# Kernel tuning notes

Measured on AMD Instinct MI355X. Metric: run time of the kernel, lower is better.

Reference implementation:

```python
import jax, jax.numpy as jnp
import numpy as np

B, D, K = 32, 20000, 16
HH, EH, L, DH = 128, 256, 32, 128


def setup_inputs() -> dict:
    key = jax.random.key(0)
    ks = jax.random.split(key, 16)
    g = lambda k, shape, fan_in: jax.random.normal(k, shape, jnp.float32) / np.sqrt(fan_in)
    return {
        "x": jax.random.normal(ks[0], (B, D), jnp.float32),
        "mask": jax.random.randint(ks[1], (B, D), 0, 2, jnp.int32),
        # encoder feature embedding/bias (shared with decoder)
        "F_embed": jax.random.normal(ks[2], (D, K), jnp.float32),
        "f_bias": jnp.zeros((D, 1), jnp.float32),
        # h_layer: Linear(1+K+1 -> HH), Linear(HH -> K)
        "W1": g(ks[3], (2 + K, HH), 2 + K), "b1": jnp.zeros((HH,), jnp.float32),
        "W2": g(ks[4], (HH, K), HH), "b2": jnp.zeros((K,), jnp.float32),
        # encoder_mlp: Linear(K -> EH), Linear(EH -> 2L)
        "We1": g(ks[5], (K, EH), K), "be1": jnp.zeros((EH,), jnp.float32),
        "We2": g(ks[6], (EH, 2 * L), EH), "be2": jnp.zeros((2 * L,), jnp.float32),
        # z_processor: Linear(L -> DH)
        "Wz": g(ks[7], (L, DH), L), "bz": jnp.zeros((DH,), jnp.float32),
        # j_layer: Linear(DH+K+1 -> DH), Linear(DH -> 1)
        "Wj1": g(ks[8], (DH + K + 1, DH), DH + K + 1), "bj1": jnp.zeros((DH,), jnp.float32),
        "Wj2": g(ks[9], (DH, 1), DH), "bj2": jnp.zeros((1,), jnp.float32),
    }


def reference(x, mask, F_embed, f_bias, W1, b1, W2, b2, We1, be1, We2, be2,
              Wz, bz, Wj1, bj1, Wj2, bj2):
    relu = jax.nn.relu
    bsz = x.shape[0]
    # ---- encoder: per-feature shared h_layer ----
    # h_input = [x_j, F_j, b_j] : (B, D, 2+K)
    h_in = jnp.concatenate([
        x[:, :, None],
        jnp.broadcast_to(F_embed[None], (bsz, D, K)),
        jnp.broadcast_to(f_bias[None], (bsz, D, 1)),
    ], axis=-1)
    h = relu(h_in @ W1 + b1)          # (B, D, HH)
    h = relu(h @ W2 + b2)             # (B, D, K)
    c = jnp.sum(h * mask.astype(jnp.float32)[:, :, None], axis=1)  # (B, K)
    enc = relu(c @ We1 + be1) @ We2 + be2                          # (B, 2L)
    mu, logvar = enc[:, :L], enc[:, L:]
    # eval mode: z = mu
    z = mu
    # ---- decoder: broadcast-concat shared j_layer ----
    pz = relu(z @ Wz + bz)            # (B, DH)
    j_in = jnp.concatenate([
        jnp.broadcast_to(pz[:, None, :], (bsz, D, DH)),
        jnp.broadcast_to(F_embed[None], (bsz, D, K)),
        jnp.broadcast_to(f_bias[None], (bsz, D, 1)),
    ], axis=-1)                       # (B, D, DH+K+1)
    rec = (relu(j_in @ Wj1 + bj1) @ Wj2 + bj2)[..., 0]  # (B, D)
    return rec, mu, logvar
```

## Files before the change

kernel.cpp:

```cpp
#include <hip/hip_runtime.h>

#define Dn 20000
#define Bn 32


__global__ __launch_bounds__(256) void kA1(const float* __restrict__ F_embed,
                                           const float* __restrict__ f_bias,
                                           const float* __restrict__ W1,
                                           const float* __restrict__ b1,
                                           float* __restrict__ F1)
{
    const int t  = threadIdx.x;
    const int k  = t & 127;
    const int dl = t >> 7;
    const int d0 = blockIdx.x * 8;
    float w[17];
#pragma unroll
    for (int i = 0; i < 16; ++i) w[i] = W1[(1 + i) * 128 + k];
    w[16] = W1[17 * 128 + k];
    const float bb = b1[k];
#pragma unroll
    for (int r = 0; r < 4; ++r) {
        const int d = d0 + r * 2 + dl;
        float acc = fmaf(f_bias[d], w[16], bb);
#pragma unroll
        for (int i = 0; i < 16; ++i) acc = fmaf(F_embed[d * 16 + i], w[i], acc);
        F1[d * 128 + k] = acc;
    }
}

__global__ __launch_bounds__(256) void kA2(const float* __restrict__ F_embed,
                                           const float* __restrict__ f_bias,
                                           const float* __restrict__ Wj1,
                                           float* __restrict__ FjT)
{
    const int d  = blockIdx.x * 256 + threadIdx.x;
    const int kg = blockIdx.y * 8;
    if (d >= Dn) return;
    const float4* fe4 = (const float4*)(F_embed + d * 16);
    float fe[16];
    {
        float4 a = fe4[0], b = fe4[1], c = fe4[2], e = fe4[3];
        fe[0]=a.x; fe[1]=a.y; fe[2]=a.z; fe[3]=a.w;
        fe[4]=b.x; fe[5]=b.y; fe[6]=b.z; fe[7]=b.w;
        fe[8]=c.x; fe[9]=c.y; fe[10]=c.z; fe[11]=c.w;
        fe[12]=e.x; fe[13]=e.y; fe[14]=e.z; fe[15]=e.w;
    }
    const float fb = f_bias[d];
#pragma unroll
    for (int j = 0; j < 8; ++j) {
        const int k = kg + j;
        float acc = fb * Wj1[144 * 128 + k];
#pragma unroll
        for (int i = 0; i < 16; ++i) acc = fmaf(fe[i], Wj1[(128 + i) * 128 + k], acc);
        FjT[k * Dn + d] = acc;
    }
}

__global__ __launch_bounds__(256) void kB(const float* __restrict__ x,
                                          const int* __restrict__ mask,
                                          const float* __restrict__ F1,
                                          const float* __restrict__ W1,
                                          const float* __restrict__ W2,
                                          const float* __restrict__ b2,
                                          float* __restrict__ partial)
{
    const int t   = threadIdx.x;
    const int b   = t & 31;
    const int dsl = t >> 5;
    const int d   = blockIdx.x * 8 + dsl;

    const float xv = x[b * Dn + d];
    const float m  = (float)mask[b * Dn + d];

    float acc[16];
#pragma unroll
    for (int j = 0; j < 16; ++j) acc[j] = 0.f;

    const float4* f14 = (const float4*)(F1 + d * 128);
#pragma unroll 8
    for (int k4 = 0; k4 < 32; ++k4) {
        const float4 f = f14[k4];
        const float h0 = fmaxf(fmaf(xv, W1[k4 * 4 + 0], f.x), 0.f);
        const float h1 = fmaxf(fmaf(xv, W1[k4 * 4 + 1], f.y), 0.f);
        const float h2 = fmaxf(fmaf(xv, W1[k4 * 4 + 2], f.z), 0.f);
        const float h3 = fmaxf(fmaf(xv, W1[k4 * 4 + 3], f.w), 0.f);
#pragma unroll
        for (int j = 0; j < 16; ++j) {
            float a = acc[j];
            a = fmaf(h0, W2[(k4 * 4 + 0) * 16 + j], a);
            a = fmaf(h1, W2[(k4 * 4 + 1) * 16 + j], a);
            a = fmaf(h2, W2[(k4 * 4 + 2) * 16 + j], a);
            a = fmaf(h3, W2[(k4 * 4 + 3) * 16 + j], a);
            acc[j] = a;
        }
    }
#pragma unroll
    for (int j = 0; j < 16; ++j) acc[j] = m * fmaxf(acc[j] + b2[j], 0.f);

#pragma unroll
    for (int j = 0; j < 16; ++j) acc[j] += __shfl_xor(acc[j], 32);
    __shared__ float red[4][544];
    const int wv   = t >> 6;
    const int lane = t & 63;
    if (lane < 32) {
#pragma unroll
        for (int j = 0; j < 16; ++j) red[wv][b * 17 + j] = acc[j];
    }
    __syncthreads();
    float* __restrict__ po = partial + blockIdx.x * 512;
    for (int o = t; o < 512; o += 256) {
        const int ob = o >> 4, oj = o & 15;
        const int idx = ob * 17 + oj;
        po[o] = red[0][idx] + red[1][idx] + red[2][idx] + red[3][idx];
    }
}

__global__ __launch_bounds__(256) void kR(const float* __restrict__ partial,
                                          float* __restrict__ cws)
{
    const int o  = blockIdx.x * 256 + threadIdx.x;
    const int r0 = blockIdx.y * 250;
    float s = 0.f;
#pragma unroll 5
    for (int r = 0; r < 250; ++r) s += partial[(r0 + r) * 512 + o];
    atomicAdd(cws + o, s);
}

__global__ __launch_bounds__(256) void kC(const float* __restrict__ cws,
                                          const float* __restrict__ We1,
                                          const float* __restrict__ be1,
                                          const float* __restrict__ We2,
                                          const float* __restrict__ be2,
                                          const float* __restrict__ Wz,
                                          const float* __restrict__ bz,
                                          const float* __restrict__ Wj1,
                                          const float* __restrict__ bj1,
                                          float* __restrict__ out,
                                          float* __restrict__ basews)
{
    const int b = blockIdx.x;
    const int t = threadIdx.x;
    __shared__ float cb[16];
    __shared__ float henc[256];
    __shared__ float ep[4][64];
    __shared__ float zl[32];
    __shared__ float pzl[128];
    __shared__ float jp[2][128];

    if (t < 16) cb[t] = cws[b * 16 + t];
    __syncthreads();

    {
        float a = be1[t];
#pragma unroll
        for (int i = 0; i < 16; ++i) a = fmaf(cb[i], We1[i * 256 + t], a);
        henc[t] = fmaxf(a, 0.f);
    }
    __syncthreads();

    {
        const int o = t & 63, s = t >> 6;
        float a = 0.f;
#pragma unroll 8
        for (int i = 0; i < 64; ++i) a = fmaf(henc[s * 64 + i], We2[(s * 64 + i) * 64 + o], a);
        ep[s][o] = a;
    }
    __syncthreads();
    if (t < 64) {
        const float e = be2[t] + ep[0][t] + ep[1][t] + ep[2][t] + ep[3][t];
        if (t < 32) { out[640000 + b * 32 + t] = e; zl[t] = e; }
        else        { out[641024 + b * 32 + (t - 32)] = e; }
    }
    __syncthreads();

    if (t < 128) {
        float a = bz[t];
#pragma unroll 8
        for (int i = 0; i < 32; ++i) a = fmaf(zl[i], Wz[i * 128 + t], a);
        pzl[t] = fmaxf(a, 0.f);
    }
    __syncthreads();

    {
        const int k = t & 127, s = t >> 7;
        float a = 0.f;
#pragma unroll 8
        for (int i = 0; i < 64; ++i) a = fmaf(pzl[s * 64 + i], Wj1[(s * 64 + i) * 128 + k], a);
        jp[s][k] = a;
    }
    __syncthreads();
    if (t < 128) basews[b * 128 + t] = bj1[t] + jp[0][t] + jp[1][t];
}

__global__ __launch_bounds__(256) void kD(const float* __restrict__ FjT,
                                          const float* __restrict__ basews,
                                          const float* __restrict__ Wj2,
                                          const float* __restrict__ bj2,
                                          float* __restrict__ rec)
{
    const int d  = blockIdx.x * 256 + threadIdx.x;
    const int bq = blockIdx.y * 4;
    if (d >= Dn) return;
    const float* __restrict__ bA = basews + (bq + 0) * 128;
    const float* __restrict__ bB = basews + (bq + 1) * 128;
    const float* __restrict__ bC = basews + (bq + 2) * 128;
    const float* __restrict__ bD = basews + (bq + 3) * 128;
    float a0 = 0.f, a1 = 0.f, a2 = 0.f, a3 = 0.f;
#pragma unroll 8
    for (int k = 0; k < 128; ++k) {
        const float fj = FjT[k * Dn + d];
        const float w  = Wj2[k];
        a0 = fmaf(fmaxf(fj + bA[k], 0.f), w, a0);
        a1 = fmaf(fmaxf(fj + bB[k], 0.f), w, a1);
        a2 = fmaf(fmaxf(fj + bC[k], 0.f), w, a2);
        a3 = fmaf(fmaxf(fj + bD[k], 0.f), w, a3);
    }
    const float bj = bj2[0];
    rec[(bq + 0) * Dn + d] = a0 + bj;
    rec[(bq + 1) * Dn + d] = a1 + bj;
    rec[(bq + 2) * Dn + d] = a2 + bj;
    rec[(bq + 3) * Dn + d] = a3 + bj;
}

extern "C" void kernel_launch(void* const* d_in, const int* in_sizes, int n_in,
                              void* d_out, int out_size, void* d_ws, size_t ws_size,
                              hipStream_t stream)
{
    const float* x       = (const float*)d_in[0];
    const int*   mask    = (const int*)d_in[1];
    const float* F_embed = (const float*)d_in[2];
    const float* f_bias  = (const float*)d_in[3];
    const float* W1      = (const float*)d_in[4];
    const float* b1      = (const float*)d_in[5];
    const float* W2      = (const float*)d_in[6];
    const float* b2      = (const float*)d_in[7];
    const float* We1     = (const float*)d_in[8];
    const float* be1     = (const float*)d_in[9];
    const float* We2     = (const float*)d_in[10];
    const float* be2     = (const float*)d_in[11];
    const float* Wz      = (const float*)d_in[12];
    const float* bz      = (const float*)d_in[13];
    const float* Wj1     = (const float*)d_in[14];
    const float* bj1     = (const float*)d_in[15];
    const float* Wj2     = (const float*)d_in[16];
    const float* bj2     = (const float*)d_in[17];
    float* out = (float*)d_out;
    float* ws  = (float*)d_ws;

    float* F1      = ws;
    float* FjT     = ws + 2560000;
    float* partial = ws + 2560000;
    float* cws     = ws + 5120000;
    float* basews  = ws + 5120512;

    hipMemsetAsync(cws, 0, 512 * sizeof(float), stream);
    kA1<<<2500, 256, 0, stream>>>(F_embed, f_bias, W1, b1, F1);
    kB<<<2500, 256, 0, stream>>>(x, mask, F1, W1, W2, b2, partial);
    kR<<<dim3(2, 10), 256, 0, stream>>>(partial, cws);
    kC<<<32, 256, 0, stream>>>(cws, We1, be1, We2, be2, Wz, bz, Wj1, bj1, out, basews);
    kA2<<<dim3(79, 16), 256, 0, stream>>>(F_embed, f_bias, Wj1, FjT);
    kD<<<dim3(79, 8), 256, 0, stream>>>(FjT, basews, Wj2, bj2, out);
}
```

Baseline: 189.9 us.

## Use bf16 MFMA for encoder h-layer second matmul in kB

Rewrites the encoder kernel kB so the HH->K second layer runs on bf16 16x16x32 MFMA instructions instead of scalar FP32 FMAs. Each block now covers 16 features with x and mask staged in shared memory, so the grid and the kR reduction extents are halved. This removes most of the scalar FMA work in the largest compute stage, at the cost of bf16 rounding of the hidden activations and W2.

```diff
diff --git a/kernel.cpp b/kernel.cpp
--- a/kernel.cpp
+++ b/kernel.cpp
@@ -1,7 +1,16 @@
 #include <hip/hip_runtime.h>
+#include <hip/hip_bf16.h>
 
 #define Dn 20000
 #define Bn 32
+
+typedef short bf8_t __attribute__((ext_vector_type(8)));
+typedef float f32x4 __attribute__((ext_vector_type(4)));
+
+static __device__ __forceinline__ short f2bf(float f) {
+    __hip_bfloat16 h = __float2bfloat16(f);
+    return __builtin_bit_cast(short, h);
+}
 
 
 __global__ __launch_bounds__(256) void kA1(const float* __restrict__ F_embed,
@@ -65,65 +74,98 @@
                                           const float* __restrict__ b2,
                                           float* __restrict__ partial)
 {
-    const int t   = threadIdx.x;
-    const int b   = t & 31;
-    const int dsl = t >> 5;
-    const int d   = blockIdx.x * 8 + dsl;
-
-    const float xv = x[b * Dn + d];
-    const float m  = (float)mask[b * Dn + d];
-
-    float acc[16];
-#pragma unroll
-    for (int j = 0; j < 16; ++j) acc[j] = 0.f;
-
-    const float4* f14 = (const float4*)(F1 + d * 128);
-#pragma unroll 8
-    for (int k4 = 0; k4 < 32; ++k4) {
-        const float4 f = f14[k4];
-        const float h0 = fmaxf(fmaf(xv, W1[k4 * 4 + 0], f.x), 0.f);
-        const float h1 = fmaxf(fmaf(xv, W1[k4 * 4 + 1], f.y), 0.f);
-        const float h2 = fmaxf(fmaf(xv, W1[k4 * 4 + 2], f.z), 0.f);
-        const float h3 = fmaxf(fmaf(xv, W1[k4 * 4 + 3], f.w), 0.f);
-#pragma unroll
-        for (int j = 0; j < 16; ++j) {
-            float a = acc[j];
-            a = fmaf(h0, W2[(k4 * 4 + 0) * 16 + j], a);
-            a = fmaf(h1, W2[(k4 * 4 + 1) * 16 + j], a);
-            a = fmaf(h2, W2[(k4 * 4 + 2) * 16 + j], a);
-            a = fmaf(h3, W2[(k4 * 4 + 3) * 16 + j], a);
-            acc[j] = a;
+    const int t = threadIdx.x;
+    const int w = t >> 6;
+    const int l = t & 63;
+    const int bhalf = w & 1;
+    const int dsub  = w >> 1;
+    const int d0 = blockIdx.x * 16;
+
+    __shared__ float xs[528];
+    __shared__ float ms[528];
+    __shared__ float red[512];
+
+    const int ko = (l >> 4) * 8;
+    float w1f[4][8];
+#pragma unroll
+    for (int s = 0; s < 4; ++s)
+#pragma unroll
+        for (int e = 0; e < 8; ++e) w1f[s][e] = W1[s * 32 + ko + e];
+    bf8_t bfr[4];
+#pragma unroll
+    for (int s = 0; s < 4; ++s)
+#pragma unroll
+        for (int e = 0; e < 8; ++e) bfr[s][e] = f2bf(W2[(s * 32 + ko + e) * 16 + (l & 15)]);
+    const float b2v = b2[l & 15];
+
+#pragma unroll
+    for (int i = 0; i < 2; ++i) {
+        const int idx = t + i * 256;
+        const int dl = idx & 15, b = idx >> 4;
+        xs[dl * 33 + b] = x[b * Dn + d0 + dl];
+        ms[dl * 33 + b] = (float)mask[b * Dn + d0 + dl];
+    }
+    __syncthreads();
+
+    f32x4 cacc = {0.f, 0.f, 0.f, 0.f};
+    const float xoff = 0.f;
+    (void)xoff;
+    for (int i = 0; i < 8; ++i) {
+        const int dl = dsub * 8 + i;
+        const int d  = d0 + dl;
+        const float xv = xs[dl * 33 + bhalf * 16 + (l & 15)];
+        f32x4 acc = {0.f, 0.f, 0.f, 0.f};
+        const float* __restrict__ f1p = F1 + (size_t)d * 128 + ko;
+#pragma unroll
+        for (int s = 0; s < 4; ++s) {
+            const float4 fa = *(const float4*)(f1p + s * 32);
+            const float4 fb = *(const float4*)(f1p + s * 32 + 4);
+            bf8_t af;
+            af[0] = f2bf(fmaxf(fmaf(xv, w1f[s][0], fa.x), 0.f));
+            af[1] = f2bf(fmaxf(fmaf(xv, w1f[s][1], fa.y), 0.f));
+            af[2] = f2bf(fmaxf(fmaf(xv, w1f[s][2], fa.z), 0.f));
+            af[3] = f2bf(fmaxf(fmaf(xv, w1f[s][3], fa.w), 0.f));
+            af[4] = f2bf(fmaxf(fmaf(xv, w1f[s][4], fb.x), 0.f));
+            af[5] = f2bf(fmaxf(fmaf(xv, w1f[s][5], fb.y), 0.f));
+            af[6] = f2bf(fmaxf(fmaf(xv, w1f[s][6], fb.z), 0.f));
+            af[7] = f2bf(fmaxf(fmaf(xv, w1f[s][7], fb.w), 0.f));
+            acc = __builtin_amdgcn_mfma_f32_16x16x32_bf16(af, bfr[s], acc, 0, 0, 0);
         }
-    }
-#pragma unroll
-    for (int j = 0; j < 16; ++j) acc[j] = m * fmaxf(acc[j] + b2[j], 0.f);
-
-#pragma unroll
-    for (int j = 0; j < 16; ++j) acc[j] += __shfl_xor(acc[j], 32);
-    __shared__ float red[4][544];
-    const int wv   = t >> 6;
-    const int lane = t & 63;
-    if (lane < 32) {
-#pragma unroll
-        for (int j = 0; j < 16; ++j) red[wv][b * 17 + j] = acc[j];
+#pragma unroll
+        for (int r = 0; r < 4; ++r) {
+            const float mvr = ms[dl * 33 + bhalf * 16 + (l >> 4) * 4 + r];
+            cacc[r] = fmaf(mvr, fmaxf(acc[r] + b2v, 0.f), cacc[r]);
+        }
+    }
+
+    const int base = bhalf * 256 + (l >> 4) * 64 + (l & 15);
+    if (dsub == 0) {
+        red[base]      = cacc[0];
+        red[base + 16] = cacc[1];
+        red[base + 32] = cacc[2];
+        red[base + 48] = cacc[3];
+    }
+    __syncthreads();
+    if (dsub == 1) {
+        red[base]      += cacc[0];
+        red[base + 16] += cacc[1];
+        red[base + 32] += cacc[2];
+        red[base + 48] += cacc[3];
     }
     __syncthreads();
     float* __restrict__ po = partial + blockIdx.x * 512;
-    for (int o = t; o < 512; o += 256) {
-        const int ob = o >> 4, oj = o & 15;
-        const int idx = ob * 17 + oj;
-        po[o] = red[0][idx] + red[1][idx] + red[2][idx] + red[3][idx];
-    }
+    po[t]       = red[t];
+    po[t + 256] = red[t + 256];
 }
 
 __global__ __launch_bounds__(256) void kR(const float* __restrict__ partial,
                                           float* __restrict__ cws)
 {
     const int o  = blockIdx.x * 256 + threadIdx.x;
-    const int r0 = blockIdx.y * 250;
+    const int r0 = blockIdx.y * 125;
     float s = 0.f;
 #pragma unroll 5
-    for (int r = 0; r < 250; ++r) s += partial[(r0 + r) * 512 + o];
+    for (int r = 0; r < 125; ++r) s += partial[(r0 + r) * 512 + o];
     atomicAdd(cws + o, s);
 }
 
@@ -256,7 +298,7 @@
 
     hipMemsetAsync(cws, 0, 512 * sizeof(float), stream);
     kA1<<<2500, 256, 0, stream>>>(F_embed, f_bias, W1, b1, F1);
-    kB<<<2500, 256, 0, stream>>>(x, mask, F1, W1, W2, b2, partial);
+    kB<<<1250, 256, 0, stream>>>(x, mask, F1, W1, W2, b2, partial);
     kR<<<dim3(2, 10), 256, 0, stream>>>(partial, cws);
     kC<<<32, 256, 0, stream>>>(cws, We1, be1, We2, be2, Wz, bz, Wj1, bj1, out, basews);
     kA2<<<dim3(79, 16), 256, 0, stream>>>(F_embed, f_bias, Wj1, FjT);
```

New measurement: 159.4 us. 16.0% less time.
